# Performance work log

Hardware: AMD Instinct MI355X
Metric: run time of the kernel (lower is better)

The kernel has to match this reference:

```python
import jax, jax.numpy as jnp
import numpy as np

NEG_SLOPE = 0.2  # LeakyReLU slope from the module


def setup_inputs() -> dict:
    key = jax.random.key(0)
    k1, k2, k3, k4, k5 = jax.random.split(key, 5)
    B, N, H = 8, 1024, 512
    node_features = jax.random.normal(k1, (B, N, H), dtype=jnp.float32)
    adjacency_matrix = jax.random.randint(k2, (B, N, N), 0, 2, dtype=jnp.int32)
    # attn_linear: Linear(2H, 1). Split weight into src/dst halves (same math as
    # applying it to concat([x_i, x_j])): score_ij = x_i.a_src + x_j.a_dst + b.
    scale = 1.0 / np.sqrt(2 * H)
    attn_w_src = jax.random.uniform(k3, (H,), jnp.float32, -scale, scale)
    attn_w_dst = jax.random.uniform(k4, (H,), jnp.float32, -scale, scale)
    attn_b = jax.random.uniform(k5, (1,), jnp.float32, -scale, scale)
    return {"node_features": node_features, "adjacency_matrix": adjacency_matrix,
            "attn_w_src": attn_w_src, "attn_w_dst": attn_w_dst, "attn_b": attn_b}


def reference(node_features, adjacency_matrix, attn_w_src, attn_w_dst, attn_b):
    B, N, H = node_features.shape
    # Decomposed additive scores: [B,N,1] + [B,1,N] + b  -> [B,N,N]
    s_src = jnp.einsum('bnh,h->bn', node_features, attn_w_src)
    s_dst = jnp.einsum('bnh,h->bn', node_features, attn_w_dst)
    scores = s_src[:, :, None] + s_dst[:, None, :] + attn_b[0]
    scores = jax.nn.leaky_relu(scores, negative_slope=NEG_SLOPE)
    # adjacency + self loops; mask where zero
    adj = adjacency_matrix.astype(jnp.float32) + jnp.eye(N, dtype=jnp.float32)[None]
    scores = jnp.where(adj == 0, -jnp.inf, scores)
    attn = jax.nn.softmax(scores, axis=-1)
    # dropout is identity in eval mode
    return jnp.einsum('bij,bjh->bih', attn, node_features)
```

## Files before the change

kernel.cpp:

```cpp
#include <hip/hip_runtime.h>
#include <hip/hip_bf16.h>

#define BB 8
#define NN 1024
#define HH 512
#define NEG 0.2f

typedef float f32x4 __attribute__((ext_vector_type(4)));
typedef short bf16x8 __attribute__((ext_vector_type(8)));
typedef unsigned int u32;

__device__ __forceinline__ unsigned short f2bf(float f) {
    union { float f; u32 u; } a; a.f = f;
    u32 u = a.u;
    u += 0x7fffu + ((u >> 16) & 1u);
    return (unsigned short)(u >> 16);
}

__device__ __forceinline__ void gload16(const void* g, void* l) {
    __builtin_amdgcn_global_load_lds(
        (const __attribute__((address_space(1))) unsigned int*)g,
        (__attribute__((address_space(3))) unsigned int*)l, 16, 0, 0);
}

__global__ __launch_bounds__(256) void prep_kernel(
    const float* __restrict__ x, const float* __restrict__ wsrc,
    const float* __restrict__ wdst, float* __restrict__ ssrc,
    float* __restrict__ sdst, unsigned short* __restrict__ xt)
{
    __shared__ __align__(16) unsigned short lt[16][528];

    int bid = blockIdx.x;
    int b = bid & 7;
    int j0 = (bid >> 3) * 16;
    int t = threadIdx.x;
    int r = t >> 4;
    int hb = (t & 15) * 32;

    const float* xrow = x + ((size_t)b * NN + j0 + r) * HH + hb;
    float psrc = 0.f, pdst = 0.f;
    #pragma unroll
    for (int q = 0; q < 8; ++q) {
        f32x4 v = *(const f32x4*)(xrow + q * 4);
        f32x4 a = *(const f32x4*)(wsrc + hb + q * 4);
        f32x4 d = *(const f32x4*)(wdst + hb + q * 4);
        psrc += v[0]*a[0] + v[1]*a[1] + v[2]*a[2] + v[3]*a[3];
        pdst += v[0]*d[0] + v[1]*d[1] + v[2]*d[2] + v[3]*d[3];
        u32 lo = (u32)f2bf(v[0]) | ((u32)f2bf(v[1]) << 16);
        u32 hi = (u32)f2bf(v[2]) | ((u32)f2bf(v[3]) << 16);
        *(u32*)&lt[r][hb + q*4 + 0] = lo;
        *(u32*)&lt[r][hb + q*4 + 2] = hi;
    }
    #pragma unroll
    for (int k = 1; k < 16; k <<= 1) {
        psrc += __shfl_xor(psrc, k);
        pdst += __shfl_xor(pdst, k);
    }
    if ((t & 15) == 0) {
        ssrc[b * NN + j0 + r] = psrc;
        sdst[b * NN + j0 + r] = pdst;
    }
    __syncthreads();

    #pragma unroll
    for (int hh = 0; hh < 2; ++hh) {
        int h = hh * 256 + t;
        unsigned short v[16];
        #pragma unroll
        for (int rr = 0; rr < 16; ++rr) v[rr] = lt[rr][h];
        unsigned short* dst = xt + ((size_t)b * HH + h) * NN + j0;
        #pragma unroll
        for (int q = 0; q < 2; ++q) {
            bf16x8 pk;
            #pragma unroll
            for (int e = 0; e < 8; ++e) pk[e] = (short)v[q*8 + e];
            *(bf16x8*)(dst + q * 8) = pk;
        }
    }
}

__global__ __launch_bounds__(256) void softmax_kernel(
    const float* __restrict__ ssrc, const float* __restrict__ sdst,
    const int* __restrict__ adj, const float* __restrict__ bptr,
    unsigned short* __restrict__ P)
{
    __shared__ __align__(16) float sd[NN];

    int bid = blockIdx.x;
    int b = bid & 7;
    int r0 = (bid >> 3) * 4;
    int t = threadIdx.x;
    int lane = t & 63;
    int w = t >> 6;

    *(f32x4*)&sd[t * 4] = *(const f32x4*)&sdst[b * NN + t * 4];
    __syncthreads();

    int ig = r0 + w;
    float si = ssrc[b * NN + ig] + bptr[0];
    const int* arow = adj + ((size_t)b * NN + ig) * NN;

    float sc[16];
    float m = -1e30f;
    #pragma unroll
    for (int it = 0; it < 4; ++it) {
        int j = it * 256 + lane * 4;
        int4 a4 = *(const int4*)(arow + j);
        f32x4 sv = *(const f32x4*)&sd[j];
        float s0 = si + sv[0]; s0 = s0 > 0.f ? s0 : NEG * s0;
        float s1 = si + sv[1]; s1 = s1 > 0.f ? s1 : NEG * s1;
        float s2 = si + sv[2]; s2 = s2 > 0.f ? s2 : NEG * s2;
        float s3 = si + sv[3]; s3 = s3 > 0.f ? s3 : NEG * s3;
        sc[it*4+0] = (a4.x != 0 || (j + 0) == ig) ? s0 : -1e30f;
        sc[it*4+1] = (a4.y != 0 || (j + 1) == ig) ? s1 : -1e30f;
        sc[it*4+2] = (a4.z != 0 || (j + 2) == ig) ? s2 : -1e30f;
        sc[it*4+3] = (a4.w != 0 || (j + 3) == ig) ? s3 : -1e30f;
        m = fmaxf(m, fmaxf(fmaxf(sc[it*4+0], sc[it*4+1]), fmaxf(sc[it*4+2], sc[it*4+3])));
    }
    #pragma unroll
    for (int k = 1; k < 64; k <<= 1) m = fmaxf(m, __shfl_xor(m, k));
    float sum = 0.f;
    #pragma unroll
    for (int k = 0; k < 16; ++k) { float e = __expf(sc[k] - m); sc[k] = e; sum += e; }
    #pragma unroll
    for (int k = 1; k < 64; k <<= 1) sum += __shfl_xor(sum, k);
    float inv = 1.f / sum;

    unsigned short* prow = P + ((size_t)b * NN + ig) * NN;
    #pragma unroll
    for (int it = 0; it < 4; ++it) {
        int j = it * 256 + lane * 4;
        u32 lo = (u32)f2bf(sc[it*4+0] * inv) | ((u32)f2bf(sc[it*4+1] * inv) << 16);
        u32 hi = (u32)f2bf(sc[it*4+2] * inv) | ((u32)f2bf(sc[it*4+3] * inv) << 16);
        *(uint2*)(prow + j) = make_uint2(lo, hi);
    }
}

__global__ __launch_bounds__(512) void pv_kernel(
    const unsigned short* __restrict__ P, const unsigned short* __restrict__ xt,
    float* __restrict__ out)
{
    __shared__ __align__(16) unsigned short As[128 * 64];
    __shared__ __align__(16) unsigned short Bs[128 * 64];

    int bid = blockIdx.x;
    int b = bid & 7;
    int tt = bid >> 3;
    int h0 = (tt & 3) * 128;
    int i0 = (tt >> 2) * 128;
    int t = threadIdx.x;
    int lane = t & 63;
    int w = t >> 6;
    int wm = w & 3;
    int wn = w >> 2;
    int g = lane >> 4;
    int ln = lane & 15;

    int row0 = t >> 3;
    int c = t & 7;
    int sj = (c ^ (row0 & 7)) * 8;
    const unsigned short* gA0 = xt + ((size_t)(b * HH + h0 + row0)) * NN + sj;
    const unsigned short* gA1 = xt + ((size_t)(b * HH + h0 + row0 + 64)) * NN + sj;
    const unsigned short* gB0 = P + ((size_t)(b * NN + i0 + row0)) * NN + sj;
    const unsigned short* gB1 = P + ((size_t)(b * NN + i0 + row0 + 64)) * NN + sj;
    unsigned short* lA0 = As + t * 8;
    unsigned short* lA1 = As + 4096 + t * 8;
    unsigned short* lB0 = Bs + t * 8;
    unsigned short* lB1 = Bs + 4096 + t * 8;

    const char* pa[2][2];
    #pragma unroll
    for (int ma = 0; ma < 2; ++ma) {
        int row = wm * 32 + ma * 16 + ln;
        #pragma unroll
        for (int kk = 0; kk < 2; ++kk)
            pa[ma][kk] = (const char*)As + ((row * 128 + kk * 64 + g * 16) ^ ((row & 7) << 4));
    }
    const char* pb[4][2];
    #pragma unroll
    for (int nb = 0; nb < 4; ++nb) {
        int row = wn * 64 + nb * 16 + ln;
        #pragma unroll
        for (int kk = 0; kk < 2; ++kk)
            pb[nb][kk] = (const char*)Bs + ((row * 128 + kk * 64 + g * 16) ^ ((row & 7) << 4));
    }

    f32x4 acc[2][4];
    #pragma unroll
    for (int ma = 0; ma < 2; ++ma)
        #pragma unroll
        for (int nb = 0; nb < 4; ++nb)
            acc[ma][nb] = (f32x4){0.f, 0.f, 0.f, 0.f};

    for (int js = 0; js < 16; ++js) {
        int joff = js * 64;
        gload16(gA0 + joff, lA0);
        gload16(gA1 + joff, lA1);
        gload16(gB0 + joff, lB0);
        gload16(gB1 + joff, lB1);
        __syncthreads();

        bf16x8 af[2][2], bfr[4][2];
        #pragma unroll
        for (int ma = 0; ma < 2; ++ma)
            #pragma unroll
            for (int kk = 0; kk < 2; ++kk)
                af[ma][kk] = *(const bf16x8*)pa[ma][kk];
        #pragma unroll
        for (int nb = 0; nb < 4; ++nb)
            #pragma unroll
            for (int kk = 0; kk < 2; ++kk)
                bfr[nb][kk] = *(const bf16x8*)pb[nb][kk];

        #pragma unroll
        for (int kk = 0; kk < 2; ++kk)
            #pragma unroll
            for (int ma = 0; ma < 2; ++ma)
                #pragma unroll
                for (int nb = 0; nb < 4; ++nb)
                    acc[ma][nb] = __builtin_amdgcn_mfma_f32_16x16x32_bf16(af[ma][kk], bfr[nb][kk], acc[ma][nb], 0, 0, 0);

        __syncthreads();
    }

    #pragma unroll
    for (int nb = 0; nb < 4; ++nb) {
        int i = i0 + wn * 64 + nb * 16 + ln;
        #pragma unroll
        for (int ma = 0; ma < 2; ++ma) {
            float* dst = out + ((size_t)(b * NN + i)) * HH + h0 + wm * 32 + ma * 16 + g * 4;
            *(f32x4*)dst = acc[ma][nb];
        }
    }
}

extern "C" void kernel_launch(void* const* d_in, const int* in_sizes, int n_in,
                              void* d_out, int out_size, void* d_ws, size_t ws_size,
                              hipStream_t stream) {
    const float* x    = (const float*)d_in[0];
    const int*   adj  = (const int*)d_in[1];
    const float* wsrc = (const float*)d_in[2];
    const float* wdst = (const float*)d_in[3];
    const float* bias = (const float*)d_in[4];
    float* out = (float*)d_out;

    float* ssrc = (float*)d_ws;
    float* sdst = ssrc + BB * NN;
    unsigned short* xt = (unsigned short*)(sdst + BB * NN);
    unsigned short* P  = xt + (size_t)BB * HH * NN;

    prep_kernel<<<dim3(BB * (NN / 16)), dim3(256), 0, stream>>>(x, wsrc, wdst, ssrc, sdst, xt);
    softmax_kernel<<<dim3(BB * NN / 4), dim3(256), 0, stream>>>(ssrc, sdst, adj, bias, P);
    pv_kernel<<<dim3(BB * 4 * 8), dim3(512), 0, stream>>>(P, xt, out);
}
```

Measured before the change: 43.42 us.

## Double-buffer PV GEMM with smaller i-tiles and widen prep transpose blocks

The PV GEMM now double-buffers its LDS tiles so the global-to-LDS loads for the next k-slice are issued before computing the current one. Its i-tile shrinks from 128 to 64 rows, which doubles the grid to 512 blocks for better CU occupancy across the device. The prep kernel handles 32 rows per 512-thread block with a coalesced h-interleaved read pattern, and the transpose writes 64-byte runs instead of 32-byte ones. The cost is less operand reuse per block in the GEMM and more LDS per block.

```diff
diff --git a/kernel.cpp b/kernel.cpp
--- a/kernel.cpp
+++ b/kernel.cpp
@@ -23,59 +23,56 @@
         (__attribute__((address_space(3))) unsigned int*)l, 16, 0, 0);
 }
 
-__global__ __launch_bounds__(256) void prep_kernel(
+__global__ __launch_bounds__(512) void prep_kernel(
     const float* __restrict__ x, const float* __restrict__ wsrc,
     const float* __restrict__ wdst, float* __restrict__ ssrc,
     float* __restrict__ sdst, unsigned short* __restrict__ xt)
 {
-    __shared__ __align__(16) unsigned short lt[16][528];
+    __shared__ __align__(16) unsigned short lt[32][520];
 
     int bid = blockIdx.x;
     int b = bid & 7;
-    int j0 = (bid >> 3) * 16;
+    int j0 = (bid >> 3) * 32;
     int t = threadIdx.x;
     int r = t >> 4;
-    int hb = (t & 15) * 32;
-
-    const float* xrow = x + ((size_t)b * NN + j0 + r) * HH + hb;
+    int l = t & 15;
+
+    const float* xrow = x + ((size_t)b * NN + j0 + r) * HH;
     float psrc = 0.f, pdst = 0.f;
     #pragma unroll
     for (int q = 0; q < 8; ++q) {
-        f32x4 v = *(const f32x4*)(xrow + q * 4);
-        f32x4 a = *(const f32x4*)(wsrc + hb + q * 4);
-        f32x4 d = *(const f32x4*)(wdst + hb + q * 4);
+        int h = q * 64 + l * 4;
+        f32x4 v = *(const f32x4*)(xrow + h);
+        f32x4 a = *(const f32x4*)(wsrc + h);
+        f32x4 d = *(const f32x4*)(wdst + h);
         psrc += v[0]*a[0] + v[1]*a[1] + v[2]*a[2] + v[3]*a[3];
         pdst += v[0]*d[0] + v[1]*d[1] + v[2]*d[2] + v[3]*d[3];
         u32 lo = (u32)f2bf(v[0]) | ((u32)f2bf(v[1]) << 16);
         u32 hi = (u32)f2bf(v[2]) | ((u32)f2bf(v[3]) << 16);
-        *(u32*)&lt[r][hb + q*4 + 0] = lo;
-        *(u32*)&lt[r][hb + q*4 + 2] = hi;
+        *(u32*)&lt[r][h + 0] = lo;
+        *(u32*)&lt[r][h + 2] = hi;
     }
     #pragma unroll
     for (int k = 1; k < 16; k <<= 1) {
         psrc += __shfl_xor(psrc, k);
         pdst += __shfl_xor(pdst, k);
     }
-    if ((t & 15) == 0) {
+    if (l == 0) {
         ssrc[b * NN + j0 + r] = psrc;
         sdst[b * NN + j0 + r] = pdst;
     }
     __syncthreads();
 
-    #pragma unroll
-    for (int hh = 0; hh < 2; ++hh) {
-        int h = hh * 256 + t;
-        unsigned short v[16];
-        #pragma unroll
-        for (int rr = 0; rr < 16; ++rr) v[rr] = lt[rr][h];
-        unsigned short* dst = xt + ((size_t)b * HH + h) * NN + j0;
-        #pragma unroll
-        for (int q = 0; q < 2; ++q) {
-            bf16x8 pk;
-            #pragma unroll
-            for (int e = 0; e < 8; ++e) pk[e] = (short)v[q*8 + e];
-            *(bf16x8*)(dst + q * 8) = pk;
-        }
+    unsigned short v[32];
+    #pragma unroll
+    for (int rr = 0; rr < 32; ++rr) v[rr] = lt[rr][t];
+    unsigned short* dst = xt + ((size_t)b * HH + t) * NN + j0;
+    #pragma unroll
+    for (int q = 0; q < 4; ++q) {
+        bf16x8 pk;
+        #pragma unroll
+        for (int e = 0; e < 8; ++e) pk[e] = (short)v[q*8 + e];
+        *(bf16x8*)(dst + q * 8) = pk;
     }
 }
 
@@ -140,14 +137,14 @@
     const unsigned short* __restrict__ P, const unsigned short* __restrict__ xt,
     float* __restrict__ out)
 {
-    __shared__ __align__(16) unsigned short As[128 * 64];
-    __shared__ __align__(16) unsigned short Bs[128 * 64];
+    __shared__ __align__(16) unsigned short As[2 * 128 * 64];
+    __shared__ __align__(16) unsigned short Bs[2 * 64 * 64];
 
     int bid = blockIdx.x;
     int b = bid & 7;
     int tt = bid >> 3;
     int h0 = (tt & 3) * 128;
-    int i0 = (tt >> 2) * 128;
+    int i0 = (tt >> 2) * 64;
     int t = threadIdx.x;
     int lane = t & 63;
     int w = t >> 6;
@@ -160,13 +157,11 @@
     int c = t & 7;
     int sj = (c ^ (row0 & 7)) * 8;
     const unsigned short* gA0 = xt + ((size_t)(b * HH + h0 + row0)) * NN + sj;
-    const unsigned short* gA1 = xt + ((size_t)(b * HH + h0 + row0 + 64)) * NN + sj;
+    const unsigned short* gA1 = gA0 + (size_t)64 * NN;
     const unsigned short* gB0 = P + ((size_t)(b * NN + i0 + row0)) * NN + sj;
-    const unsigned short* gB1 = P + ((size_t)(b * NN + i0 + row0 + 64)) * NN + sj;
     unsigned short* lA0 = As + t * 8;
     unsigned short* lA1 = As + 4096 + t * 8;
     unsigned short* lB0 = Bs + t * 8;
-    unsigned short* lB1 = Bs + 4096 + t * 8;
 
     const char* pa[2][2];
     #pragma unroll
@@ -176,56 +171,63 @@
         for (int kk = 0; kk < 2; ++kk)
             pa[ma][kk] = (const char*)As + ((row * 128 + kk * 64 + g * 16) ^ ((row & 7) << 4));
     }
-    const char* pb[4][2];
-    #pragma unroll
-    for (int nb = 0; nb < 4; ++nb) {
-        int row = wn * 64 + nb * 16 + ln;
+    const char* pb[2][2];
+    #pragma unroll
+    for (int nb = 0; nb < 2; ++nb) {
+        int row = wn * 32 + nb * 16 + ln;
         #pragma unroll
         for (int kk = 0; kk < 2; ++kk)
             pb[nb][kk] = (const char*)Bs + ((row * 128 + kk * 64 + g * 16) ^ ((row & 7) << 4));
     }
 
-    f32x4 acc[2][4];
+    f32x4 acc[2][2];
     #pragma unroll
     for (int ma = 0; ma < 2; ++ma)
         #pragma unroll
-        for (int nb = 0; nb < 4; ++nb)
+        for (int nb = 0; nb < 2; ++nb)
             acc[ma][nb] = (f32x4){0.f, 0.f, 0.f, 0.f};
 
-    for (int js = 0; js < 16; ++js) {
+    auto stage = [&](int p, int js) {
         int joff = js * 64;
-        gload16(gA0 + joff, lA0);
-        gload16(gA1 + joff, lA1);
-        gload16(gB0 + joff, lB0);
-        gload16(gB1 + joff, lB1);
-        __syncthreads();
-
-        bf16x8 af[2][2], bfr[4][2];
+        gload16(gA0 + joff, lA0 + p * 8192);
+        gload16(gA1 + joff, lA1 + p * 8192);
+        gload16(gB0 + joff, lB0 + p * 4096);
+    };
+    auto compute = [&](int ofsA, int ofsB) {
+        bf16x8 af[2][2], bfr[2][2];
         #pragma unroll
         for (int ma = 0; ma < 2; ++ma)
             #pragma unroll
             for (int kk = 0; kk < 2; ++kk)
-                af[ma][kk] = *(const bf16x8*)pa[ma][kk];
-        #pragma unroll
-        for (int nb = 0; nb < 4; ++nb)
+                af[ma][kk] = *(const bf16x8*)(pa[ma][kk] + ofsA);
+        #pragma unroll
+        for (int nb = 0; nb < 2; ++nb)
             #pragma unroll
             for (int kk = 0; kk < 2; ++kk)
-                bfr[nb][kk] = *(const bf16x8*)pb[nb][kk];
-
+                bfr[nb][kk] = *(const bf16x8*)(pb[nb][kk] + ofsB);
         #pragma unroll
         for (int kk = 0; kk < 2; ++kk)
             #pragma unroll
             for (int ma = 0; ma < 2; ++ma)
                 #pragma unroll
-                for (int nb = 0; nb < 4; ++nb)
+                for (int nb = 0; nb < 2; ++nb)
                     acc[ma][nb] = __builtin_amdgcn_mfma_f32_16x16x32_bf16(af[ma][kk], bfr[nb][kk], acc[ma][nb], 0, 0, 0);
-
+    };
+
+    stage(0, 0);
+    __syncthreads();
+    for (int js = 0; js < 16; js += 2) {
+        if (js + 1 < 16) stage(1, js + 1);
+        compute(0, 0);
         __syncthreads();
-    }
-
-    #pragma unroll
-    for (int nb = 0; nb < 4; ++nb) {
-        int i = i0 + wn * 64 + nb * 16 + ln;
+        if (js + 2 < 16) stage(0, js + 2);
+        compute(16384, 8192);
+        __syncthreads();
+    }
+
+    #pragma unroll
+    for (int nb = 0; nb < 2; ++nb) {
+        int i = i0 + wn * 32 + nb * 16 + ln;
         #pragma unroll
         for (int ma = 0; ma < 2; ++ma) {
             float* dst = out + ((size_t)(b * NN + i)) * HH + h0 + wm * 32 + ma * 16 + g * 4;
@@ -249,7 +251,7 @@
     unsigned short* xt = (unsigned short*)(sdst + BB * NN);
     unsigned short* P  = xt + (size_t)BB * HH * NN;
 
-    prep_kernel<<<dim3(BB * (NN / 16)), dim3(256), 0, stream>>>(x, wsrc, wdst, ssrc, sdst, xt);
+    prep_kernel<<<dim3(BB * (NN / 32)), dim3(512), 0, stream>>>(x, wsrc, wdst, ssrc, sdst, xt);
     softmax_kernel<<<dim3(BB * NN / 4), dim3(256), 0, stream>>>(ssrc, sdst, adj, bias, P);
-    pv_kernel<<<dim3(BB * 4 * 8), dim3(512), 0, stream>>>(P, xt, out);
-}
+    pv_kernel<<<dim3(BB * 4 * 16), dim3(512), 0, stream>>>(P, xt, out);
+}
```

Result: faster. 38.77 us (-10.7%).
